# Kernel tuning notes

Hardware: AMD Instinct MI355X
Metric: run time of the kernel (lower is better)

The kernel has to match this reference:

```python
import jax, jax.numpy as jnp
import numpy as np
from jax import lax

CAPACITY_FACTOR = 1.0

def setup_inputs() -> dict:
    key = jax.random.key(0)
    k1, k2 = jax.random.split(key)
    x = jax.random.normal(k1, (16384, 4096), dtype=jnp.float32)
    wg = jax.random.normal(k2, (128, 4096), dtype=jnp.float32) * (1.0 / np.sqrt(4096))
    return {"x": x, "wg": wg}


def reference(x, wg):
    # logits: [T, E]
    logits = jnp.einsum('td,ed->te', x, wg)
    T, E = logits.shape
    capacity = 2 * int(CAPACITY_FACTOR * ((T + E - 1) // E))  # static python int

    # top-2 expert indices per token
    _, top2 = lax.top_k(logits, 2)           # [T, 2]
    idx1, idx2 = top2[:, 0], top2[:, 1]       # [T]

    mask1 = jax.nn.one_hot(idx1, E, dtype=jnp.int32)  # [T, E]
    mask2 = jax.nn.one_hot(idx2, E, dtype=jnp.int32)

    gates = jax.nn.softmax(logits, axis=1)    # [T, E]
    gates1_s = jnp.sum(gates * mask1, axis=1)  # [T]
    gates2_s = jnp.sum(gates * mask2, axis=1)

    # per-expert running position (cumsum over tokens)
    locations1 = jnp.cumsum(mask1, axis=0) - 1
    locations2 = jnp.cumsum(mask2, axis=0) - 1 + jnp.sum(mask1, axis=0, keepdims=True)

    # drop tokens over capacity
    mask1 = mask1 * (locations1 < capacity).astype(jnp.int32)
    mask2 = mask2 * (locations2 < capacity).astype(jnp.int32)

    locations1_s = jnp.sum(locations1 * mask1, axis=1)  # [T]
    locations2_s = jnp.sum(locations2 * mask2, axis=1)

    # load-balancing aux loss (float32 branch of original)
    me = jnp.sum(gates, axis=0)                       # [E]
    ce = jnp.sum(mask1.astype(gates.dtype), axis=0)   # [E] (post-capacity mask)
    l_aux = jnp.sum(me * ce) * (E / (T * T))

    return (l_aux, capacity, E,
            idx1.astype(jnp.int32), idx2.astype(jnp.int32),
            locations1_s.astype(jnp.int32), locations2_s.astype(jnp.int32),
            gates1_s, gates2_s)
```

## Files before the change

kernel.cpp:

```cpp
#include <hip/hip_runtime.h>

typedef _Float16 half8  __attribute__((ext_vector_type(8)));
typedef float    f32x4  __attribute__((ext_vector_type(4)));
typedef float    f32x16 __attribute__((ext_vector_type(16)));

#define T_TOK 16384
#define D_DIM 4096
#define E_EXP 128
#define CAP   256
#define BM    32
#define NT    32

#define A_BUF   8192
#define A_PIPE  16384
#define SMEM_SZ 33792

__global__ __launch_bounds__(256) void prep_wt(
    const float* __restrict__ wg, _Float16* __restrict__ wt)
{
    const int t = blockIdx.x * 256 + threadIdx.x;
    const int c = t & 3;
    const int e = (t >> 2) & 127;
    const int s = t >> 9;

    const float* src = wg + (size_t)e * D_DIM + s * 32 + c * 8;
    const f32x4 v0 = *reinterpret_cast<const f32x4*>(src);
    const f32x4 v1 = *reinterpret_cast<const f32x4*>(src + 4);

    half8 h, m;
#pragma unroll
    for (int j = 0; j < 4; j++) {
        float sv = v0[j] * 64.0f;
        _Float16 hh = (_Float16)sv;
        h[j] = hh; m[j] = (_Float16)(sv - (float)hh);
        sv = v1[j] * 64.0f;
        hh = (_Float16)sv;
        h[4 + j] = hh; m[4 + j] = (_Float16)(sv - (float)hh);
    }
    _Float16* dst = wt + (size_t)s * 8192 + e * 32 + c * 8;
    *reinterpret_cast<half8*>(dst)        = h;
    *reinterpret_cast<half8*>(dst + 4096) = m;
}

__global__ __launch_bounds__(512, 4) void gemm_gate(
    const float* __restrict__ x, const _Float16* __restrict__ wt,
    float* __restrict__ out, float* __restrict__ me, int* __restrict__ cnt1)
{
    __shared__ char smem[SMEM_SZ];

    const int tid  = threadIdx.x;
    const int row0 = blockIdx.x * BM;
    const int lane = tid & 63;
    const int w    = tid >> 6;
    const int kp   = w >> 2;
    const int wl   = w & 3;
    const int col  = lane & 31;
    const int k8   = lane >> 5;

    const int sp = tid >> 8;
    const int sr = (tid >> 3) & 31;
    const int sg = tid & 7;
    const float* xA = x + (size_t)(row0 + sr) * D_DIM + sp * 2048 + sg * 8;
    const int awr_h = sp * A_PIPE + sr * 256 + ((sg ^ (sr & 7)) * 16);

    const char* const ard = smem + kp * A_PIPE + col * 256;
    const int rsw = col & 7;

    const _Float16* const wtB =
        wt + (size_t)(kp * 64) * 8192 + (wl * 32 + col) * 32 + k8 * 8;

    f32x16 acc = (f32x16)0.0f;

#define LOAD_BS(Bh, Bm, t, k)                                                 \
    {                                                                         \
        const _Float16* bp = wtB +                                            \
            (size_t)((2 * (t) + ((k) >> 1)) & 63) * 8192 + ((k) & 1) * 16;    \
        Bh = *reinterpret_cast<const half8*>(bp);                             \
        Bm = *reinterpret_cast<const half8*>(bp + 4096);                      \
    }

#define CONV_WRITE(a0, a1, buf)                                               \
    {                                                                         \
        half8 h, m;                                                           \
        _Pragma("unroll") for (int j = 0; j < 4; j++) {                       \
            _Float16 hh = (_Float16)a0[j];                                    \
            h[j] = hh; m[j] = (_Float16)(a0[j] - (float)hh);                  \
            hh = (_Float16)a1[j];                                             \
            h[4 + j] = hh; m[4 + j] = (_Float16)(a1[j] - (float)hh);          \
        }                                                                     \
        char* const wb = smem + (buf) * A_BUF + awr_h;                        \
        *reinterpret_cast<half8*>(wb)       = h;                              \
        *reinterpret_cast<half8*>(wb + 128) = m;                              \
    }

#define BAR()                                                                 \
    asm volatile("s_waitcnt lgkmcnt(0)" ::: "memory");                        \
    __builtin_amdgcn_sched_barrier(0);                                        \
    __builtin_amdgcn_s_barrier();                                             \
    __builtin_amdgcn_sched_barrier(0);

#define SUB(cur, k, Bh, Bm)                                                   \
    {                                                                         \
        const char* ab = ard + (cur) * A_BUF + ((((k) * 2 + k8) ^ rsw) * 16); \
        const half8 Ah = *reinterpret_cast<const half8*>(ab);                 \
        const half8 Am = *reinterpret_cast<const half8*>(ab + 128);           \
        acc = __builtin_amdgcn_mfma_f32_32x32x16_f16(Am, Bh, acc, 0, 0, 0);   \
        acc = __builtin_amdgcn_mfma_f32_32x32x16_f16(Ah, Bm, acc, 0, 0, 0);   \
        acc = __builtin_amdgcn_mfma_f32_32x32x16_f16(Ah, Bh, acc, 0, 0, 0);   \
    }

#define STEP(cur, t)                                                          \
    {                                                                         \
        LOAD_BS(B1h, B1m, t, 1);                                              \
        LOAD_BS(B2h, B2m, t, 2);                                              \
        LOAD_BS(B3h, B3m, t, 3);                                              \
        __builtin_amdgcn_sched_barrier(0);                                    \
        const int kn = (((t) + 1) & (NT - 1)) * 64;                           \
        const f32x4 a0 = *reinterpret_cast<const f32x4*>(xA + kn);            \
        const f32x4 a1 = *reinterpret_cast<const f32x4*>(xA + kn + 4);        \
        __builtin_amdgcn_sched_barrier(0);                                    \
        SUB(cur, 0, B0h, B0m);                                                \
        LOAD_BS(B0h, B0m, (t) + 1, 0);                                        \
        SUB(cur, 1, B1h, B1m);                                                \
        SUB(cur, 2, B2h, B2m);                                                \
        SUB(cur, 3, B3h, B3m);                                                \
        CONV_WRITE(a0, a1, (cur) ^ 1);                                        \
        BAR();                                                                \
    }

    half8 B0h, B0m, B1h, B1m, B2h, B2m, B3h, B3m;

    {
        const f32x4 a0 = *reinterpret_cast<const f32x4*>(xA);
        const f32x4 a1 = *reinterpret_cast<const f32x4*>(xA + 4);
        LOAD_BS(B0h, B0m, 0, 0);
        CONV_WRITE(a0, a1, 0);
        BAR();
    }

    for (int t = 0; t < NT; t += 2) {
        STEP(0, t);
        STEP(1, t + 1);
    }

#undef STEP
#undef SUB
#undef BAR
#undef CONV_WRITE
#undef LOAD_BS

    float* lg = reinterpret_cast<float*>(smem);
    if (kp == 1) {
#pragma unroll
        for (int reg = 0; reg < 16; reg++) {
            const int row = (reg & 3) + 8 * (reg >> 2) + 4 * k8;
            lg[row * 129 + wl * 32 + col] = acc[reg] * 0.015625f;
        }
    }
    __syncthreads();
    if (kp == 0) {
#pragma unroll
        for (int reg = 0; reg < 16; reg++) {
            const int row = (reg & 3) + 8 * (reg >> 2) + 4 * k8;
            lg[row * 129 + wl * 32 + col] += acc[reg] * 0.015625f;
        }
    }
    __syncthreads();

    float* sm1v  = reinterpret_cast<float*>(smem + 20480);
    float* sinvv = sm1v + 32;

    if (tid < BM) {
        const int r = tid;
        const int t = row0 + r;
        float m1 = -1e30f, m2 = -1e30f;
        int   i1 = 0, i2 = 0;
        for (int e = 0; e < E_EXP; e++) {
            const float v = lg[r * 129 + e];
            if (v > m1)      { m2 = m1; i2 = i1; m1 = v; i1 = e; }
            else if (v > m2) { m2 = v; i2 = e; }
        }
        float s = 0.0f;
        for (int e = 0; e < E_EXP; e++) s += __expf(lg[r * 129 + e] - m1);
        const float inv = 1.0f / s;

        out[3 + 0 * T_TOK + t] = (float)i1;
        out[3 + 1 * T_TOK + t] = (float)i2;
        out[3 + 4 * T_TOK + t] = inv;
        out[3 + 5 * T_TOK + t] = __expf(m2 - m1) * inv;
        atomicAdd(&cnt1[i1], 1);
        sm1v[r]  = m1;
        sinvv[r] = inv;
    }
    __syncthreads();

    {
        const int r  = tid & 31;
        const int e0 = (tid >> 5) * 8;
        const float m1 = sm1v[r], inv = sinvv[r];
#pragma unroll
        for (int j = 0; j < 8; j++)
            lg[r * 129 + e0 + j] = __expf(lg[r * 129 + e0 + j] - m1) * inv;
    }
    __syncthreads();

    if (tid < E_EXP) {
        float s = 0.0f;
        for (int r = 0; r < BM; r++) s += lg[r * 129 + tid];
        atomicAdd(&me[tid], s);
    }
}

__global__ __launch_bounds__(1024) void rank_kernel(
    float* __restrict__ out, const int* __restrict__ cnt1)
{
    const int  e      = blockIdx.x & 127;
    const bool second = blockIdx.x >= 128;
    const int  tid    = threadIdx.x;
    const int  lane   = tid & 63;
    const int  w      = tid >> 6;

    __shared__ int wtot[16];

    const float* idxA = out + 3 + (second ? T_TOK : 0);
    float* loc = out + 3 + (second ? 3 * T_TOK : 2 * T_TOK);

    const unsigned long long below = (1ull << lane) - 1ull;
    int base = second ? cnt1[e] : 0;

    for (int t0 = 0; t0 < T_TOK; t0 += 1024) {
        const int t = t0 + tid;
        const int f = ((int)idxA[t] == e);
        const unsigned long long m = __ballot(f);
        const int pre = __popcll(m & below);
        const int tot = __popcll(m);
        if (lane == 0) wtot[w] = tot;
        __syncthreads();
        int off = 0, all = 0;
#pragma unroll
        for (int i = 0; i < 16; i++) {
            const int v = wtot[i];
            if (i < w) off += v;
            all += v;
        }
        if (f) {
            const int rank = base + off + pre;
            loc[t] = (rank < CAP) ? (float)rank : 0.0f;
        }
        base += all;
        __syncthreads();
    }
}

__global__ __launch_bounds__(128) void finalize_kernel(
    const float* __restrict__ me, const int* __restrict__ cnt1,
    float* __restrict__ out)
{
    __shared__ float red[2];
    const int tid = threadIdx.x;
    const int c = cnt1[tid];
    float p = me[tid] * (float)((c < CAP) ? c : CAP);
#pragma unroll
    for (int o = 32; o > 0; o >>= 1) p += __shfl_down(p, o);
    if ((tid & 63) == 0) red[tid >> 6] = p;
    __syncthreads();
    if (tid == 0) {
        const float tot = red[0] + red[1];
        out[0] = tot * ((float)E_EXP / ((float)T_TOK * (float)T_TOK));
        out[1] = (float)CAP;
        out[2] = (float)E_EXP;
    }
}

extern "C" void kernel_launch(void* const* d_in, const int* in_sizes, int n_in,
                              void* d_out, int out_size, void* d_ws, size_t ws_size,
                              hipStream_t stream)
{
    const float* x  = (const float*)d_in[0];
    const float* wg = (const float*)d_in[1];
    float* out = (float*)d_out;

    float* me   = (float*)d_ws;
    int*   cnt1 = (int*)((char*)d_ws + 512);
    _Float16* wt = (_Float16*)((char*)d_ws + 1024);

    hipMemsetAsync(d_ws, 0, 1024, stream);
    prep_wt<<<256, 256, 0, stream>>>(wg, wt);
    gemm_gate<<<T_TOK / BM, 512, 0, stream>>>(x, wt, out, me, cnt1);
    rank_kernel<<<2 * E_EXP, 1024, 0, stream>>>(out, cnt1);
    finalize_kernel<<<1, 128, 0, stream>>>(me, cnt1, out);
}
```

Measured before the change: 130.7 us.

## Split-K GEMM into partial-logit kernel with 64-row tiles and separate gating kernel

Each GEMM block now covers 64 rows instead of 32, with two accumulators per wave, so every loaded B fragment is reused across two MFMA row tiles. The K dimension is also split across two blocks (grid stays 512). The partial logits go to a global workspace, and a new gate kernel sums them and runs top-2, softmax and the expert-sum reduction. This halves weight traffic per token and cuts B loads relative to MFMA work. In exchange it adds a global round trip for the logits, an extra launch, and 64KB of LDS per block, which may limit occupancy.

```diff
diff --git a/kernel.cpp b/kernel.cpp
--- a/kernel.cpp
+++ b/kernel.cpp
@@ -1,19 +1,18 @@
 #include <hip/hip_runtime.h>
 
-typedef _Float16 half8  __attribute__((ext_vector_type(8)));
-typedef float    f32x4  __attribute__((ext_vector_type(4)));
+typedef _Float16 half8 __attribute__((ext_vector_type(8)));
+typedef float    f32x4 __attribute__((ext_vector_type(4)));
 typedef float    f32x16 __attribute__((ext_vector_type(16)));
 
 #define T_TOK 16384
 #define D_DIM 4096
 #define E_EXP 128
 #define CAP   256
-#define BM    32
-#define NT    32
-
-#define A_BUF   8192
-#define A_PIPE  16384
-#define SMEM_SZ 33792
+#define BM    64
+#define NT    16
+
+#define A_BUF 16384
+#define A_SP  32768
 
 __global__ __launch_bounds__(256) void prep_wt(
     const float* __restrict__ wg, _Float16* __restrict__ wt)
@@ -42,55 +41,67 @@
     *reinterpret_cast<half8*>(dst + 4096) = m;
 }
 
-__global__ __launch_bounds__(512, 4) void gemm_gate(
+__global__ __launch_bounds__(512, 4) void gemm_partial(
     const float* __restrict__ x, const _Float16* __restrict__ wt,
-    float* __restrict__ out, float* __restrict__ me, int* __restrict__ cnt1)
-{
-    __shared__ char smem[SMEM_SZ];
+    float* __restrict__ lgw)
+{
+    __shared__ char smem[2 * A_SP];
 
     const int tid  = threadIdx.x;
-    const int row0 = blockIdx.x * BM;
+    const int tile = blockIdx.x & 255;
+    const int kh   = blockIdx.x >> 8;
+    const int row0 = tile * BM;
     const int lane = tid & 63;
     const int w    = tid >> 6;
-    const int kp   = w >> 2;
-    const int wl   = w & 3;
+    const int spw  = w >> 2;
+    const int cg   = w & 3;
     const int col  = lane & 31;
     const int k8   = lane >> 5;
 
     const int sp = tid >> 8;
-    const int sr = (tid >> 3) & 31;
-    const int sg = tid & 7;
-    const float* xA = x + (size_t)(row0 + sr) * D_DIM + sp * 2048 + sg * 8;
-    const int awr_h = sp * A_PIPE + sr * 256 + ((sg ^ (sr & 7)) * 16);
-
-    const char* const ard = smem + kp * A_PIPE + col * 256;
+    const int ro = tid & 255;
+    const int sr = ro >> 2;
+    const int sg = ro & 3;
+    const float* xA = x + (size_t)(row0 + sr) * D_DIM +
+                      kh * 2048 + sp * 1024 + sg * 16;
+    const int aw  = sp * A_SP + sr * 256;
+    const int c0  = ((sg * 2    ) ^ (sr & 7)) * 16;
+    const int c1  = ((sg * 2 + 1) ^ (sr & 7)) * 16;
+
+    const char* const ard = smem + spw * A_SP + col * 256;
     const int rsw = col & 7;
 
     const _Float16* const wtB =
-        wt + (size_t)(kp * 64) * 8192 + (wl * 32 + col) * 32 + k8 * 8;
-
-    f32x16 acc = (f32x16)0.0f;
+        wt + (size_t)(kh * 64 + spw * 32) * 8192 + (cg * 32 + col) * 32 + k8 * 8;
+
+    f32x16 acc0 = (f32x16)0.0f, acc1 = (f32x16)0.0f;
 
 #define LOAD_BS(Bh, Bm, t, k)                                                 \
     {                                                                         \
         const _Float16* bp = wtB +                                            \
-            (size_t)((2 * (t) + ((k) >> 1)) & 63) * 8192 + ((k) & 1) * 16;    \
+            (size_t)((2 * (t) + ((k) >> 1)) & 31) * 8192 + ((k) & 1) * 16;    \
         Bh = *reinterpret_cast<const half8*>(bp);                             \
         Bm = *reinterpret_cast<const half8*>(bp + 4096);                      \
     }
 
-#define CONV_WRITE(a0, a1, buf)                                               \
+#define CONV_WRITE(a0v, a1v, a2v, a3v, buf)                                   \
     {                                                                         \
-        half8 h, m;                                                           \
+        half8 h0, m0, h1, m1;                                                 \
         _Pragma("unroll") for (int j = 0; j < 4; j++) {                       \
-            _Float16 hh = (_Float16)a0[j];                                    \
-            h[j] = hh; m[j] = (_Float16)(a0[j] - (float)hh);                  \
-            hh = (_Float16)a1[j];                                             \
-            h[4 + j] = hh; m[4 + j] = (_Float16)(a1[j] - (float)hh);          \
+            _Float16 hh = (_Float16)a0v[j];                                   \
+            h0[j] = hh; m0[j] = (_Float16)(a0v[j] - (float)hh);               \
+            hh = (_Float16)a1v[j];                                            \
+            h0[4 + j] = hh; m0[4 + j] = (_Float16)(a1v[j] - (float)hh);       \
+            hh = (_Float16)a2v[j];                                            \
+            h1[j] = hh; m1[j] = (_Float16)(a2v[j] - (float)hh);               \
+            hh = (_Float16)a3v[j];                                            \
+            h1[4 + j] = hh; m1[4 + j] = (_Float16)(a3v[j] - (float)hh);       \
         }                                                                     \
-        char* const wb = smem + (buf) * A_BUF + awr_h;                        \
-        *reinterpret_cast<half8*>(wb)       = h;                              \
-        *reinterpret_cast<half8*>(wb + 128) = m;                              \
+        char* const wb = smem + aw + (buf) * A_BUF;                           \
+        *reinterpret_cast<half8*>(wb + c0)       = h0;                        \
+        *reinterpret_cast<half8*>(wb + c1)       = h1;                        \
+        *reinterpret_cast<half8*>(wb + c0 + 128) = m0;                        \
+        *reinterpret_cast<half8*>(wb + c1 + 128) = m1;                        \
     }
 
 #define BAR()                                                                 \
@@ -101,12 +112,19 @@
 
 #define SUB(cur, k, Bh, Bm)                                                   \
     {                                                                         \
-        const char* ab = ard + (cur) * A_BUF + ((((k) * 2 + k8) ^ rsw) * 16); \
-        const half8 Ah = *reinterpret_cast<const half8*>(ab);                 \
-        const half8 Am = *reinterpret_cast<const half8*>(ab + 128);           \
-        acc = __builtin_amdgcn_mfma_f32_32x32x16_f16(Am, Bh, acc, 0, 0, 0);   \
-        acc = __builtin_amdgcn_mfma_f32_32x32x16_f16(Ah, Bm, acc, 0, 0, 0);   \
-        acc = __builtin_amdgcn_mfma_f32_32x32x16_f16(Ah, Bh, acc, 0, 0, 0);   \
+        const int ch = ((((k) * 2 + k8) ^ rsw) * 16);                         \
+        const char* ab0 = ard + (cur) * A_BUF + ch;                           \
+        const char* ab1 = ab0 + 32 * 256;                                     \
+        const half8 Ah0 = *reinterpret_cast<const half8*>(ab0);               \
+        const half8 Am0 = *reinterpret_cast<const half8*>(ab0 + 128);         \
+        const half8 Ah1 = *reinterpret_cast<const half8*>(ab1);               \
+        const half8 Am1 = *reinterpret_cast<const half8*>(ab1 + 128);         \
+        acc0 = __builtin_amdgcn_mfma_f32_32x32x16_f16(Am0, Bh, acc0, 0,0,0);  \
+        acc1 = __builtin_amdgcn_mfma_f32_32x32x16_f16(Am1, Bh, acc1, 0,0,0);  \
+        acc0 = __builtin_amdgcn_mfma_f32_32x32x16_f16(Ah0, Bm, acc0, 0,0,0);  \
+        acc1 = __builtin_amdgcn_mfma_f32_32x32x16_f16(Ah1, Bm, acc1, 0,0,0);  \
+        acc0 = __builtin_amdgcn_mfma_f32_32x32x16_f16(Ah0, Bh, acc0, 0,0,0);  \
+        acc1 = __builtin_amdgcn_mfma_f32_32x32x16_f16(Ah1, Bh, acc1, 0,0,0);  \
     }
 
 #define STEP(cur, t)                                                          \
@@ -116,15 +134,17 @@
         LOAD_BS(B3h, B3m, t, 3);                                              \
         __builtin_amdgcn_sched_barrier(0);                                    \
         const int kn = (((t) + 1) & (NT - 1)) * 64;                           \
-        const f32x4 a0 = *reinterpret_cast<const f32x4*>(xA + kn);            \
-        const f32x4 a1 = *reinterpret_cast<const f32x4*>(xA + kn + 4);        \
+        const f32x4 av0 = *reinterpret_cast<const f32x4*>(xA + kn);           \
+        const f32x4 av1 = *reinterpret_cast<const f32x4*>(xA + kn + 4);       \
+        const f32x4 av2 = *reinterpret_cast<const f32x4*>(xA + kn + 8);       \
+        const f32x4 av3 = *reinterpret_cast<const f32x4*>(xA + kn + 12);      \
         __builtin_amdgcn_sched_barrier(0);                                    \
         SUB(cur, 0, B0h, B0m);                                                \
         LOAD_BS(B0h, B0m, (t) + 1, 0);                                        \
         SUB(cur, 1, B1h, B1m);                                                \
         SUB(cur, 2, B2h, B2m);                                                \
         SUB(cur, 3, B3h, B3m);                                                \
-        CONV_WRITE(a0, a1, (cur) ^ 1);                                        \
+        CONV_WRITE(av0, av1, av2, av3, (cur) ^ 1);                            \
         BAR();                                                                \
     }
 
@@ -133,8 +153,10 @@
     {
         const f32x4 a0 = *reinterpret_cast<const f32x4*>(xA);
         const f32x4 a1 = *reinterpret_cast<const f32x4*>(xA + 4);
+        const f32x4 a2 = *reinterpret_cast<const f32x4*>(xA + 8);
+        const f32x4 a3 = *reinterpret_cast<const f32x4*>(xA + 12);
         LOAD_BS(B0h, B0m, 0, 0);
-        CONV_WRITE(a0, a1, 0);
+        CONV_WRITE(a0, a1, a2, a3, 0);
         BAR();
     }
 
@@ -149,26 +171,55 @@
 #undef CONV_WRITE
 #undef LOAD_BS
 
-    float* lg = reinterpret_cast<float*>(smem);
-    if (kp == 1) {
+    float* mg = reinterpret_cast<float*>(smem);
+    __syncthreads();
+    if (spw == 1) {
+        float* b = mg + cg * 32 + col;
 #pragma unroll
         for (int reg = 0; reg < 16; reg++) {
             const int row = (reg & 3) + 8 * (reg >> 2) + 4 * k8;
-            lg[row * 129 + wl * 32 + col] = acc[reg] * 0.015625f;
-        }
-    }
-    __syncthreads();
-    if (kp == 0) {
+            b[row * 128]        = acc0[reg];
+            b[(row + 32) * 128] = acc1[reg];
+        }
+    }
+    __syncthreads();
+    if (spw == 0) {
+        float* dst = lgw + ((size_t)kh * 256 + tile) * 8192 + cg * 32 + col;
+        const float* srcp = mg + cg * 32 + col;
 #pragma unroll
         for (int reg = 0; reg < 16; reg++) {
             const int row = (reg & 3) + 8 * (reg >> 2) + 4 * k8;
-            lg[row * 129 + wl * 32 + col] += acc[reg] * 0.015625f;
-        }
-    }
-    __syncthreads();
-
-    float* sm1v  = reinterpret_cast<float*>(smem + 20480);
-    float* sinvv = sm1v + 32;
+            dst[row * 128]        = acc0[reg] + srcp[row * 128];
+            dst[(row + 32) * 128] = acc1[reg] + srcp[(row + 32) * 128];
+        }
+    }
+}
+
+__global__ __launch_bounds__(256) void gate_kernel(
+    const float* __restrict__ lgw, float* __restrict__ out,
+    float* __restrict__ me, int* __restrict__ cnt1)
+{
+    __shared__ float lg[BM * 129];
+    __shared__ float sm1v[BM], sinvv[BM];
+
+    const int tile = blockIdx.x;
+    const int tid  = threadIdx.x;
+    const int row0 = tile * BM;
+
+    const float* p0 = lgw + (size_t)tile * 8192;
+    const float* p1 = p0 + (size_t)256 * 8192;
+
+#pragma unroll
+    for (int i = 0; i < 8; i++) {
+        const int off = i * 1024 + tid * 4;
+        const f32x4 v0 = *reinterpret_cast<const f32x4*>(p0 + off);
+        const f32x4 v1 = *reinterpret_cast<const f32x4*>(p1 + off);
+        const int r = off >> 7, c = off & 127;
+#pragma unroll
+        for (int j = 0; j < 4; j++)
+            lg[r * 129 + c + j] = (v0[j] + v1[j]) * 0.015625f;
+    }
+    __syncthreads();
 
     if (tid < BM) {
         const int r = tid;
@@ -195,11 +246,11 @@
     __syncthreads();
 
     {
-        const int r  = tid & 31;
-        const int e0 = (tid >> 5) * 8;
+        const int r  = tid >> 2;
+        const int e0 = (tid & 3) * 32;
         const float m1 = sm1v[r], inv = sinvv[r];
 #pragma unroll
-        for (int j = 0; j < 8; j++)
+        for (int j = 0; j < 32; j++)
             lg[r * 129 + e0 + j] = __expf(lg[r * 129 + e0 + j] - m1) * inv;
     }
     __syncthreads();
@@ -283,10 +334,12 @@
     float* me   = (float*)d_ws;
     int*   cnt1 = (int*)((char*)d_ws + 512);
     _Float16* wt = (_Float16*)((char*)d_ws + 1024);
+    float* lgw  = (float*)((char*)d_ws + 1024 + (size_t)2 * 1024 * 1024);
 
     hipMemsetAsync(d_ws, 0, 1024, stream);
     prep_wt<<<256, 256, 0, stream>>>(wg, wt);
-    gemm_gate<<<T_TOK / BM, 512, 0, stream>>>(x, wt, out, me, cnt1);
+    gemm_partial<<<512, 512, 0, stream>>>(x, wt, lgw);
+    gate_kernel<<<256, 256, 0, stream>>>(lgw, out, me, cnt1);
     rank_kernel<<<2 * E_EXP, 1024, 0, stream>>>(out, cnt1);
     finalize_kernel<<<1, 128, 0, stream>>>(me, cnt1, out);
 }
```

Measured after the change: 129.1 us. No clear change (-1.3%).
